# Performance work log

Measured on AMD Instinct MI355X. Metric: run time of the kernel, lower is better.

The kernel has to match this reference:

```python
import jax, jax.numpy as jnp
import numpy as np

G = 2048      # graphs
N = 48        # nodes per graph
NTOT = G * N  # 98304 total nodes
F_IN = 64
HID = 128
HEADS = 1
K = 4         # TopKPooling ratio (int -> k nodes per graph)
DEG = 8
E = NTOT * DEG
ATT = HEADS * 8  # attention pooling heads
EPS = 1e-5


def setup_inputs() -> dict:
    key = jax.random.key(0)
    ks = jax.random.split(key, 20)
    off = (jnp.arange(G, dtype=jnp.int32) * N)[:, None]
    # intra-graph random edges (source j -> target i), GATConv convention
    edge_src = (jax.random.randint(ks[0], (G, N * DEG), 0, N, dtype=jnp.int32) + off).reshape(-1)
    edge_dst = (jax.random.randint(ks[1], (G, N * DEG), 0, N, dtype=jnp.int32) + off).reshape(-1)
    batch = jnp.repeat(jnp.arange(G, dtype=jnp.int32), N)

    def w(k, shape, fan):
        return jax.random.normal(k, shape, jnp.float32) * (1.0 / np.sqrt(fan))

    HH = HEADS * HID
    return dict(
        x=jax.random.normal(ks[2], (NTOT, F_IN), jnp.float32),
        edge_src=edge_src, edge_dst=edge_dst, batch=batch,
        # GATConv 1/2/3: weight, att_src, att_dst, bias
        W1=w(ks[3], (F_IN, HH), F_IN), as1=w(ks[4], (HEADS, HID), HID), ad1=w(ks[5], (HEADS, HID), HID), b1=jnp.zeros((HH,), jnp.float32),
        W2=w(ks[6], (HH, HH), HH), as2=w(ks[7], (HEADS, HID), HID), ad2=w(ks[8], (HEADS, HID), HID), b2=jnp.zeros((HH,), jnp.float32),
        W3=w(ks[9], (HH, HH), HH), as3=w(ks[10], (HEADS, HID), HID), ad3=w(ks[11], (HEADS, HID), HID), b3=jnp.zeros((HID,), jnp.float32),
        ln1_w=jnp.ones((HH,), jnp.float32), ln1_b=jnp.zeros((HH,), jnp.float32),
        ln2_w=jnp.ones((HH,), jnp.float32), ln2_b=jnp.zeros((HH,), jnp.float32),
        ln3_w=jnp.ones((HID,), jnp.float32), ln3_b=jnp.zeros((HID,), jnp.float32),
        pool_w=w(ks[12], (HID,), HID),
        fc1_w=w(ks[13], (HID, HID), HID), fc1_b=jnp.zeros((HID,), jnp.float32),
        fc2_w=w(ks[14], (HID, ATT), HID), fc2_b=jnp.zeros((ATT,), jnp.float32),
    )


def _forward(x, edge_src, edge_dst, W1, as1, ad1, b1, W2, as2, ad2, b2,
             W3, as3, ad3, b3, ln1_w, ln1_b, ln2_w, ln2_b, ln3_w, ln3_b,
             pool_w, fc1_w, fc1_b, fc2_w, fc2_b):
    # GATConv adds self-loops
    loop = jnp.arange(NTOT, dtype=edge_src.dtype)
    src = jnp.concatenate([edge_src, loop])
    dst = jnp.concatenate([edge_dst, loop])

    def gat(h_in, W, a_s, a_d, bias, concat):
        H, C = a_s.shape
        h = (h_in @ W).reshape(NTOT, H, C)
        # e_ij = LeakyReLU(a_src . h_j + a_dst . h_i), softmax over incoming edges of i
        e = jax.nn.leaky_relu((h * a_s).sum(-1)[src] + (h * a_d).sum(-1)[dst], 0.2)  # [E', H]
        m = jax.ops.segment_max(e, dst, num_segments=NTOT)
        p = jnp.exp(e - m[dst])
        z = jax.ops.segment_sum(p, dst, num_segments=NTOT)
        alpha = p / (z[dst] + 1e-16)
        out = jax.ops.segment_sum(h[src] * alpha[:, :, None], dst, num_segments=NTOT)
        out = out.reshape(NTOT, H * C) if concat else out.mean(1)
        return out + bias

    def graph_ln(h, w, b):  # PyG LayerNorm mode='graph': normalize over nodes+channels per graph
        h3 = h.reshape(G, N, -1)
        mu = h3.mean((1, 2), keepdims=True)
        var = ((h3 - mu) ** 2).mean((1, 2), keepdims=True)
        return (((h3 - mu) / jnp.sqrt(var + EPS)) * w + b).reshape(NTOT, -1)

    h = jax.nn.relu(graph_ln(gat(x, W1, as1, ad1, b1, True), ln1_w, ln1_b))
    h = jax.nn.relu(graph_ln(gat(h, W2, as2, ad2, b2, True), ln2_w, ln2_b))
    h = graph_ln(gat(h, W3, as3, ad3, b3, False), ln3_w, ln3_b)  # [NTOT, HID]

    # TopKPooling: score = tanh(x.w/||w||), pick K nodes per graph, scale features by score
    score = jnp.tanh((h @ pool_w) / jnp.linalg.norm(pool_w))
    vals, idx = jax.lax.top_k(score.reshape(G, N), K)          # [G, K]
    h3 = h.reshape(G, N, HID)
    pooled = (jnp.take_along_axis(h3, idx[:, :, None], axis=1) * vals[:, :, None]).reshape(G, K * HID)

    # per-graph attention pooling (vectorized over the original Python loop)
    t = jnp.tanh(h3 @ fc1_w + fc1_b)                            # [G, N, HID]
    att = jax.nn.softmax(t @ fc2_w + fc2_b, axis=1)             # softmax over nodes, [G, N, ATT]
    emb = jnp.einsum('gna,gnh->gah', att, h3)                   # [G, ATT, HID]
    avg = emb.sum(-1) / ATT                                     # [G, ATT]

    return jnp.concatenate([pooled, avg], axis=1)               # [G, K*HID + ATT]


def reference(x, edge_src, edge_dst, batch, W1, as1, ad1, b1, W2, as2, ad2, b2,
              W3, as3, ad3, b3, ln1_w, ln1_b, ln2_w, ln2_b, ln3_w, ln3_b,
              pool_w, fc1_w, fc1_b, fc2_w, fc2_b):
    # batch is implicit in the uniform [G, N] layout; kept for signature fidelity
    del batch
    return _forward(x, edge_src, edge_dst, W1, as1, ad1, b1, W2, as2, ad2, b2,
                    W3, as3, ad3, b3, ln1_w, ln1_b, ln2_w, ln2_b, ln3_w, ln3_b,
                    pool_w, fc1_w, fc1_b, fc2_w, fc2_b)
```

## Files before the change

kernel.cpp:

```cpp
#include <hip/hip_runtime.h>
#include <math.h>

#define NG   2048
#define NN   48
#define FIN  64
#define HIDC 128
#define DEG  8
#define EPG  (NN*DEG)
#define NATT 8
#define KTOP 4
#define NTH  256
#define OUTW (KTOP*HIDC + NATT)

struct alignas(16) SM {
  float hA[NN*HIDC];
  float hB[NN*HIDC];
  float alpha[EPG];
  float ssrc[NN], sdst[NN], aself[NN];
  float rs[NN], sc[NN];
  float red[16];
  float valk[KTOP];
  int   idxk[KTOP];
  int   row_start[NN+1];
  int   fill[NN];
  unsigned char csr_src[EPG];
};

__device__ __forceinline__ float fast_tanh(float x) {
  float e = __expf(2.f * x);
  return 1.f - 2.f * __builtin_amdgcn_rcpf(e + 1.f);
}

template<int KD>
__device__ __forceinline__ void gemm48(const float* in, const float* __restrict__ W,
                                       int t, float acc[6][4]) {
  const int col = t & 31, row = t >> 5;
  const int c0 = col * 4, n0 = row * 6;
  #pragma unroll
  for (int i = 0; i < 6; ++i)
    #pragma unroll
    for (int j = 0; j < 4; ++j) acc[i][j] = 0.f;
  const float* wp = W + c0;
  float4 w0 = *(const float4*)(wp + 0*HIDC);
  float4 w1 = *(const float4*)(wp + 1*HIDC);
  float4 w2 = *(const float4*)(wp + 2*HIDC);
  float4 w3 = *(const float4*)(wp + 3*HIDC);
  #pragma unroll 2
  for (int kb = 0; kb < KD - 4; kb += 4) {
    const float* np = wp + (size_t)(kb + 4) * HIDC;
    float4 nw0 = *(const float4*)(np + 0*HIDC);
    float4 nw1 = *(const float4*)(np + 1*HIDC);
    float4 nw2 = *(const float4*)(np + 2*HIDC);
    float4 nw3 = *(const float4*)(np + 3*HIDC);
    #pragma unroll
    for (int i = 0; i < 6; ++i) {
      float4 h = *(const float4*)(in + (n0+i)*KD + kb);
      acc[i][0] = fmaf(h.w, w3.x, fmaf(h.z, w2.x, fmaf(h.y, w1.x, fmaf(h.x, w0.x, acc[i][0]))));
      acc[i][1] = fmaf(h.w, w3.y, fmaf(h.z, w2.y, fmaf(h.y, w1.y, fmaf(h.x, w0.y, acc[i][1]))));
      acc[i][2] = fmaf(h.w, w3.z, fmaf(h.z, w2.z, fmaf(h.y, w1.z, fmaf(h.x, w0.z, acc[i][2]))));
      acc[i][3] = fmaf(h.w, w3.w, fmaf(h.z, w2.w, fmaf(h.y, w1.w, fmaf(h.x, w0.w, acc[i][3]))));
    }
    w0 = nw0; w1 = nw1; w2 = nw2; w3 = nw3;
  }
  {
    const int kb = KD - 4;
    #pragma unroll
    for (int i = 0; i < 6; ++i) {
      float4 h = *(const float4*)(in + (n0+i)*KD + kb);
      acc[i][0] = fmaf(h.w, w3.x, fmaf(h.z, w2.x, fmaf(h.y, w1.x, fmaf(h.x, w0.x, acc[i][0]))));
      acc[i][1] = fmaf(h.w, w3.y, fmaf(h.z, w2.y, fmaf(h.y, w1.y, fmaf(h.x, w0.y, acc[i][1]))));
      acc[i][2] = fmaf(h.w, w3.z, fmaf(h.z, w2.z, fmaf(h.y, w1.z, fmaf(h.x, w0.z, acc[i][2]))));
      acc[i][3] = fmaf(h.w, w3.w, fmaf(h.z, w2.w, fmaf(h.y, w1.w, fmaf(h.x, w0.w, acc[i][3]))));
    }
  }
}

template<int KD, bool RELU>
__device__ __forceinline__ void gat_layer(SM& s, const float* in, float* hmid, float* outbuf,
                                          const float* __restrict__ W,
                                          const float* __restrict__ avs,
                                          const float* __restrict__ avd,
                                          const float* __restrict__ bias,
                                          const float* __restrict__ lnw,
                                          const float* __restrict__ lnb, int t) {
  float acc[6][4];
  gemm48<KD>(in, W, t, acc);
  const int col = t & 31, row = t >> 5, c0 = col * 4, n0 = row * 6;
  float4 asv = *(const float4*)(avs + c0);
  float4 adv = *(const float4*)(avd + c0);
  #pragma unroll
  for (int i = 0; i < 6; ++i) {
    float4 v = make_float4(acc[i][0], acc[i][1], acc[i][2], acc[i][3]);
    *(float4*)(hmid + (n0+i)*HIDC + c0) = v;
    float ps = v.x*asv.x + v.y*asv.y + v.z*asv.z + v.w*asv.w;
    float pd = v.x*adv.x + v.y*adv.y + v.z*adv.z + v.w*adv.w;
    #pragma unroll
    for (int off = 16; off > 0; off >>= 1) {
      ps += __shfl_xor(ps, off, 32);
      pd += __shfl_xor(pd, off, 32);
    }
    if (col == 0) { s.ssrc[n0+i] = ps; s.sdst[n0+i] = pd; }
  }
  __syncthreads();

  if (t < 4*NN) {
    const int n = t >> 2, l = t & 3;
    const int b0 = s.row_start[n], b1 = s.row_start[n+1];
    const float di = s.sdst[n];
    float es = s.ssrc[n] + di; es = es > 0.f ? es : 0.2f*es;
    float m = es;
    for (int q = b0 + l; q < b1; q += 4) {
      float e = s.ssrc[s.csr_src[q]] + di; e = e > 0.f ? e : 0.2f*e;
      s.alpha[q] = e;
      m = fmaxf(m, e);
    }
    m = fmaxf(m, __shfl_xor(m, 1, 4));
    m = fmaxf(m, __shfl_xor(m, 2, 4));
    float pself = expf(es - m);
    float z = (l == 0) ? pself : 0.f;
    for (int q = b0 + l; q < b1; q += 4) {
      float p = expf(s.alpha[q] - m); s.alpha[q] = p; z += p;
    }
    z += __shfl_xor(z, 1, 4);
    z += __shfl_xor(z, 2, 4);
    float inv = 1.f / (z + 1e-16f);
    for (int q = b0 + l; q < b1; q += 4) s.alpha[q] *= inv;
    if (l == 0) s.aself[n] = pself * inv;
  }
  __syncthreads();

  {
    const int cg = t & 31, rg = t >> 5;
    const float4 bc = *(const float4*)(bias + cg*4);
    const float4* hm4 = (const float4*)hmid;
    float4* ob4 = (float4*)outbuf;
    float lsum = 0.f, lsq = 0.f;
    #pragma unroll
    for (int j = 0; j < 6; ++j) {
      const int i = rg + 8*j;
      const int b0 = s.row_start[i], b1 = s.row_start[i+1];
      float4 hv = hm4[i*32 + cg];
      const float asf = s.aself[i];
      float4 av = make_float4(asf*hv.x, asf*hv.y, asf*hv.z, asf*hv.w);
      int q = b0;
      float a_nxt = 0.f; int s_nxt = 0;
      if (q < b1) { a_nxt = s.alpha[q]; s_nxt = s.csr_src[q]; }
      while (q < b1) {
        const float a = a_nxt; const int sc = s_nxt;
        ++q;
        if (q < b1) { a_nxt = s.alpha[q]; s_nxt = s.csr_src[q]; }
        float4 h4 = hm4[sc*32 + cg];
        av.x = fmaf(a, h4.x, av.x);
        av.y = fmaf(a, h4.y, av.y);
        av.z = fmaf(a, h4.z, av.z);
        av.w = fmaf(a, h4.w, av.w);
      }
      av.x += bc.x; av.y += bc.y; av.z += bc.z; av.w += bc.w;
      ob4[i*32 + cg] = av;
      lsum += av.x + av.y + av.z + av.w;
      lsq = fmaf(av.x, av.x, lsq); lsq = fmaf(av.y, av.y, lsq);
      lsq = fmaf(av.z, av.z, lsq); lsq = fmaf(av.w, av.w, lsq);
    }
    #pragma unroll
    for (int off = 32; off > 0; off >>= 1) {
      lsum += __shfl_xor(lsum, off, 64);
      lsq  += __shfl_xor(lsq,  off, 64);
    }
    const int wid = t >> 6;
    if ((t & 63) == 0) { s.red[wid] = lsum; s.red[8+wid] = lsq; }
  }
  __syncthreads();

  {
    float su = s.red[0] + s.red[1] + s.red[2] + s.red[3];
    float sq = s.red[8] + s.red[9] + s.red[10] + s.red[11];
    const float inv_n = 1.f / (NN*HIDC);
    const float mu = su * inv_n;
    const float rstd = 1.f / sqrtf(sq * inv_n - mu*mu + 1e-5f);
    const int cg = t & 31;
    const float4 wc  = *(const float4*)(lnw + cg*4);
    const float4 bcn = *(const float4*)(lnb + cg*4);
    float4* ob4 = (float4*)outbuf;
    for (int e = t; e < NN*32; e += NTH) {
      float4 v = ob4[e];
      v.x = (v.x - mu)*rstd*wc.x + bcn.x;
      v.y = (v.y - mu)*rstd*wc.y + bcn.y;
      v.z = (v.z - mu)*rstd*wc.z + bcn.z;
      v.w = (v.w - mu)*rstd*wc.w + bcn.w;
      if (RELU) {
        v.x = fmaxf(v.x, 0.f); v.y = fmaxf(v.y, 0.f);
        v.z = fmaxf(v.z, 0.f); v.w = fmaxf(v.w, 0.f);
      }
      ob4[e] = v;
    }
  }
  __syncthreads();
}

__global__ __launch_bounds__(NTH)
void gat_fused(const float* __restrict__ x,
               const int* __restrict__ edge_src, const int* __restrict__ edge_dst,
               const float* __restrict__ W1, const float* __restrict__ as1, const float* __restrict__ ad1, const float* __restrict__ b1,
               const float* __restrict__ W2, const float* __restrict__ as2, const float* __restrict__ ad2, const float* __restrict__ b2,
               const float* __restrict__ W3, const float* __restrict__ as3, const float* __restrict__ ad3, const float* __restrict__ b3,
               const float* __restrict__ ln1w, const float* __restrict__ ln1b,
               const float* __restrict__ ln2w, const float* __restrict__ ln2b,
               const float* __restrict__ ln3w, const float* __restrict__ ln3b,
               const float* __restrict__ poolw,
               const float* __restrict__ fc1w, const float* __restrict__ fc1b,
               const float* __restrict__ fc2w, const float* __restrict__ fc2b,
               float* __restrict__ out) {
  __shared__ SM s;
  const int g = blockIdx.x, t = threadIdx.x;
  const int base = g * NN;

  {
    const float4* xs = (const float4*)(x + (size_t)base*FIN);
    for (int e = t; e < NN*FIN/4; e += NTH) ((float4*)s.hA)[e] = xs[e];
  }

  if (t < NN) s.fill[t] = 0;
  __syncthreads();
  for (int e = t; e < EPG; e += NTH)
    atomicAdd(&s.fill[edge_dst[(size_t)g*EPG + e] - base], 1);
  __syncthreads();
  if (t < 64) {
    int cnt = (t < NN) ? s.fill[t] : 0;
    int xv = cnt;
    #pragma unroll
    for (int d = 1; d < 64; d <<= 1) {
      int v = __shfl_up(xv, d, 64);
      if (t >= d) xv += v;
    }
    if (t < NN) { s.row_start[t] = xv - cnt; s.fill[t] = xv - cnt; }
    if (t == NN-1) s.row_start[NN] = xv;
  }
  __syncthreads();
  for (int e = t; e < EPG; e += NTH) {
    int d  = edge_dst[(size_t)g*EPG + e] - base;
    int sl = edge_src[(size_t)g*EPG + e] - base;
    int pos = atomicAdd(&s.fill[d], 1);
    s.csr_src[pos] = (unsigned char)sl;
  }
  __syncthreads();

  gat_layer<FIN,  true >(s, s.hA, s.hB, s.hA, W1, as1, ad1, b1, ln1w, ln1b, t);
  gat_layer<HIDC, true >(s, s.hA, s.hB, s.hA, W2, as2, ad2, b2, ln2w, ln2b, t);
  gat_layer<HIDC, false>(s, s.hA, s.hB, s.hA, W3, as3, ad3, b3, ln3w, ln3b, t);

  float invnorm;
  {
    const int ln = t & 63;
    float p0 = poolw[ln], p1 = poolw[ln + 64];
    float v = p0*p0 + p1*p1;
    #pragma unroll
    for (int off = 32; off > 0; off >>= 1) v += __shfl_xor(v, off, 64);
    invnorm = 1.f / sqrtf(v);
  }

  {
    const int col = t & 31, row = t >> 5, n0 = row * 6;
    float pwv[4];
    #pragma unroll
    for (int q = 0; q < 4; ++q) pwv[q] = poolw[col + 32*q];
    #pragma unroll
    for (int i = 0; i < 6; ++i) {
      float d = 0.f, r = 0.f;
      #pragma unroll
      for (int q = 0; q < 4; ++q) {
        float v = s.hA[(n0+i)*HIDC + col + 32*q];
        d = fmaf(v, pwv[q], d); r += v;
      }
      #pragma unroll
      for (int off = 16; off > 0; off >>= 1) {
        d += __shfl_xor(d, off, 32);
        r += __shfl_xor(r, off, 32);
      }
      if (col == 0) { s.sc[n0+i] = tanhf(d * invnorm); s.rs[n0+i] = r; }
    }
  }
  __syncthreads();

  if (t < 64) {
    float cur = (t < NN) ? s.sc[t] : -1e30f;
    #pragma unroll
    for (int k = 0; k < KTOP; ++k) {
      float bv = cur; int bi = t;
      #pragma unroll
      for (int d = 1; d < 64; d <<= 1) {
        float ov = __shfl_xor(bv, d, 64);
        int   oi = __shfl_xor(bi, d, 64);
        if (ov > bv || (ov == bv && oi < bi)) { bv = ov; bi = oi; }
      }
      if (t == 0) { s.valk[k] = bv; s.idxk[k] = bi; }
      if (t == bi) cur = -1e30f;
    }
  }
  __syncthreads();

  float* og = out + (size_t)g * OUTW;
  for (int o = t; o < KTOP*HIDC; o += NTH) {
    int k = o >> 7, c = o & 127;
    og[o] = s.hA[s.idxk[k]*HIDC + c] * s.valk[k];
  }

  {
    float acc[6][4];
    gemm48<HIDC>(s.hA, fc1w, t, acc);
    const int col = t & 31, row = t >> 5, c0 = col*4, n0 = row*6;
    float4 bv = *(const float4*)(fc1b + c0);
    #pragma unroll
    for (int i = 0; i < 6; ++i) {
      float4 v;
      v.x = fast_tanh(acc[i][0] + bv.x); v.y = fast_tanh(acc[i][1] + bv.y);
      v.z = fast_tanh(acc[i][2] + bv.z); v.w = fast_tanh(acc[i][3] + bv.w);
      *(float4*)(s.hB + (n0+i)*HIDC + c0) = v;
    }
  }
  __syncthreads();

  {
    const int col = t & 31, row = t >> 5, n0 = row * 6;
    #pragma unroll
    for (int i = 0; i < 6; ++i) {
      float lg[NATT];
      #pragma unroll
      for (int a = 0; a < NATT; ++a) lg[a] = 0.f;
      #pragma unroll
      for (int q = 0; q < 4; ++q) {
        float v = s.hB[(n0+i)*HIDC + col + 32*q];
        const float* f2 = fc2w + (size_t)(col + 32*q)*NATT;
        #pragma unroll
        for (int a = 0; a < NATT; ++a) lg[a] = fmaf(v, f2[a], lg[a]);
      }
      #pragma unroll
      for (int a = 0; a < NATT; ++a) {
        #pragma unroll
        for (int off = 16; off > 0; off >>= 1) lg[a] += __shfl_xor(lg[a], off, 32);
      }
      if (col == 0) {
        #pragma unroll
        for (int a = 0; a < NATT; ++a) s.alpha[(n0+i)*NATT + a] = lg[a] + fc2b[a];
      }
    }
  }
  __syncthreads();

  {
    const int wv = t >> 6, ln = t & 63;
    #pragma unroll
    for (int aa = 0; aa < 2; ++aa) {
      const int a = wv + 4*aa;
      float lg = (ln < NN) ? s.alpha[ln*NATT + a] : -1e30f;
      float m = lg;
      #pragma unroll
      for (int off = 32; off > 0; off >>= 1) m = fmaxf(m, __shfl_xor(m, off, 64));
      float p = (ln < NN) ? expf(lg - m) : 0.f;
      float w_n = (ln < NN) ? s.rs[ln] : 0.f;
      float zz = p, acc0 = p * w_n;
      #pragma unroll
      for (int off = 32; off > 0; off >>= 1) {
        zz   += __shfl_xor(zz,   off, 64);
        acc0 += __shfl_xor(acc0, off, 64);
      }
      if (ln == 0) og[KTOP*HIDC + a] = acc0 / zz * (1.0f / NATT);
    }
  }
}

extern "C" void kernel_launch(void* const* d_in, const int* in_sizes, int n_in,
                              void* d_out, int out_size, void* d_ws, size_t ws_size,
                              hipStream_t stream) {
  (void)in_sizes; (void)n_in; (void)d_ws; (void)ws_size; (void)out_size;
  const float* x    = (const float*)d_in[0];
  const int*   esrc = (const int*)  d_in[1];
  const int*   edst = (const int*)  d_in[2];
  const float* W1   = (const float*)d_in[4];
  const float* as1  = (const float*)d_in[5];
  const float* ad1  = (const float*)d_in[6];
  const float* b1   = (const float*)d_in[7];
  const float* W2   = (const float*)d_in[8];
  const float* as2  = (const float*)d_in[9];
  const float* ad2  = (const float*)d_in[10];
  const float* b2   = (const float*)d_in[11];
  const float* W3   = (const float*)d_in[12];
  const float* as3  = (const float*)d_in[13];
  const float* ad3  = (const float*)d_in[14];
  const float* b3   = (const float*)d_in[15];
  const float* ln1w = (const float*)d_in[16];
  const float* ln1b = (const float*)d_in[17];
  const float* ln2w = (const float*)d_in[18];
  const float* ln2b = (const float*)d_in[19];
  const float* ln3w = (const float*)d_in[20];
  const float* ln3b = (const float*)d_in[21];
  const float* pw   = (const float*)d_in[22];
  const float* fc1w = (const float*)d_in[23];
  const float* fc1b = (const float*)d_in[24];
  const float* fc2w = (const float*)d_in[25];
  const float* fc2b = (const float*)d_in[26];
  float* out = (float*)d_out;

  gat_fused<<<NG, NTH, 0, stream>>>(x, esrc, edst,
                                    W1, as1, ad1, b1,
                                    W2, as2, ad2, b2,
                                    W3, as3, ad3, b3,
                                    ln1w, ln1b, ln2w, ln2b, ln3w, ln3b,
                                    pw, fc1w, fc1b, fc2w, fc2b, out);
}
```

Baseline: 246.2 us.

## Split fused GAT kernel into per-stage kernels with global workspace buffers

Replaces the single fused per-graph kernel, which held two 48x128 activation buffers in shared memory, with eight launches: CSR build, per-layer GEMM, per-layer aggregation+LayerNorm, and a pooling tail. Intermediates go through the workspace in global memory. Each kernel needs less LDS, so more blocks can be resident per CU. The cost is extra launches and global round-trips of the activations between stages. The old fused kernel is kept as a fallback when the workspace is too small.

```diff
diff --git a/kernel.cpp b/kernel.cpp
--- a/kernel.cpp
+++ b/kernel.cpp
@@ -11,6 +11,396 @@
 #define KTOP 4
 #define NTH  256
 #define OUTW (KTOP*HIDC + NATT)
+#define NTOT (NG*NN)
+
+__device__ __forceinline__ float fast_tanh(float x) {
+  float e = __expf(2.f * x);
+  return 1.f - 2.f * __builtin_amdgcn_rcpf(e + 1.f);
+}
+
+template<int KD>
+__device__ __forceinline__ void gemm48(const float* in, const float* __restrict__ W,
+                                       int t, float acc[6][4]) {
+  const int col = t & 31, row = t >> 5;
+  const int c0 = col * 4, n0 = row * 6;
+  #pragma unroll
+  for (int i = 0; i < 6; ++i)
+    #pragma unroll
+    for (int j = 0; j < 4; ++j) acc[i][j] = 0.f;
+  const float* wp = W + c0;
+  float4 w0 = *(const float4*)(wp + 0*HIDC);
+  float4 w1 = *(const float4*)(wp + 1*HIDC);
+  float4 w2 = *(const float4*)(wp + 2*HIDC);
+  float4 w3 = *(const float4*)(wp + 3*HIDC);
+  #pragma unroll 2
+  for (int kb = 0; kb < KD - 4; kb += 4) {
+    const float* np = wp + (size_t)(kb + 4) * HIDC;
+    float4 nw0 = *(const float4*)(np + 0*HIDC);
+    float4 nw1 = *(const float4*)(np + 1*HIDC);
+    float4 nw2 = *(const float4*)(np + 2*HIDC);
+    float4 nw3 = *(const float4*)(np + 3*HIDC);
+    #pragma unroll
+    for (int i = 0; i < 6; ++i) {
+      float4 h = *(const float4*)(in + (n0+i)*KD + kb);
+      acc[i][0] = fmaf(h.w, w3.x, fmaf(h.z, w2.x, fmaf(h.y, w1.x, fmaf(h.x, w0.x, acc[i][0]))));
+      acc[i][1] = fmaf(h.w, w3.y, fmaf(h.z, w2.y, fmaf(h.y, w1.y, fmaf(h.x, w0.y, acc[i][1]))));
+      acc[i][2] = fmaf(h.w, w3.z, fmaf(h.z, w2.z, fmaf(h.y, w1.z, fmaf(h.x, w0.z, acc[i][2]))));
+      acc[i][3] = fmaf(h.w, w3.w, fmaf(h.z, w2.w, fmaf(h.y, w1.w, fmaf(h.x, w0.w, acc[i][3]))));
+    }
+    w0 = nw0; w1 = nw1; w2 = nw2; w3 = nw3;
+  }
+  {
+    const int kb = KD - 4;
+    #pragma unroll
+    for (int i = 0; i < 6; ++i) {
+      float4 h = *(const float4*)(in + (n0+i)*KD + kb);
+      acc[i][0] = fmaf(h.w, w3.x, fmaf(h.z, w2.x, fmaf(h.y, w1.x, fmaf(h.x, w0.x, acc[i][0]))));
+      acc[i][1] = fmaf(h.w, w3.y, fmaf(h.z, w2.y, fmaf(h.y, w1.y, fmaf(h.x, w0.y, acc[i][1]))));
+      acc[i][2] = fmaf(h.w, w3.z, fmaf(h.z, w2.z, fmaf(h.y, w1.z, fmaf(h.x, w0.z, acc[i][2]))));
+      acc[i][3] = fmaf(h.w, w3.w, fmaf(h.z, w2.w, fmaf(h.y, w1.w, fmaf(h.x, w0.w, acc[i][3]))));
+    }
+  }
+}
+
+
+__global__ __launch_bounds__(64)
+void k_csr(const int* __restrict__ edge_src, const int* __restrict__ edge_dst,
+           int* __restrict__ grs, unsigned char* __restrict__ gcsr) {
+  __shared__ int fill[NN];
+  __shared__ int rstart[NN+1];
+  __shared__ unsigned char csr[EPG];
+  const int g = blockIdx.x, l = threadIdx.x, base = g*NN;
+  const int* ed = edge_dst + (size_t)g*EPG;
+  const int* es = edge_src + (size_t)g*EPG;
+  if (l < NN) fill[l] = 0;
+  __syncthreads();
+  #pragma unroll
+  for (int j = 0; j < EPG/64; ++j) atomicAdd(&fill[ed[j*64 + l] - base], 1);
+  __syncthreads();
+  {
+    int cnt = (l < NN) ? fill[l] : 0;
+    int xv = cnt;
+    #pragma unroll
+    for (int d = 1; d < 64; d <<= 1) {
+      int v = __shfl_up(xv, d, 64);
+      if (l >= d) xv += v;
+    }
+    if (l < NN) { rstart[l] = xv - cnt; fill[l] = xv - cnt; }
+    if (l == NN-1) rstart[NN] = xv;
+  }
+  __syncthreads();
+  #pragma unroll
+  for (int j = 0; j < EPG/64; ++j) {
+    int e = j*64 + l;
+    int pos = atomicAdd(&fill[ed[e] - base], 1);
+    csr[pos] = (unsigned char)(es[e] - base);
+  }
+  __syncthreads();
+  if (l < NN+1) grs[(size_t)g*(NN+1) + l] = rstart[l];
+  for (int j = l; j < EPG/4; j += 64)
+    ((int*)(gcsr + (size_t)g*EPG))[j] = ((const int*)csr)[j];
+}
+
+template<int KD>
+__global__ __launch_bounds__(NTH)
+void k_gemm(const float* __restrict__ hin, const float* __restrict__ W,
+            const float* __restrict__ avs, const float* __restrict__ avd,
+            float* __restrict__ msg, float* __restrict__ gss, float* __restrict__ gsd) {
+  __shared__ float hs[NN*KD];
+  const int g = blockIdx.x, t = threadIdx.x;
+  {
+    const float4* src = (const float4*)(hin + (size_t)g*NN*KD);
+    float4* dst = (float4*)hs;
+    #pragma unroll
+    for (int j = 0; j < (NN*KD/4)/NTH; ++j) dst[j*NTH + t] = src[j*NTH + t];
+  }
+  __syncthreads();
+  float acc[6][4];
+  gemm48<KD>(hs, W, t, acc);
+  const int col = t & 31, row = t >> 5, c0 = col*4, n0 = row*6;
+  float4 asv = *(const float4*)(avs + c0);
+  float4 adv = *(const float4*)(avd + c0);
+  float* mg = msg + (size_t)g*NN*HIDC;
+  #pragma unroll
+  for (int i = 0; i < 6; ++i) {
+    float4 v = make_float4(acc[i][0], acc[i][1], acc[i][2], acc[i][3]);
+    *(float4*)(mg + (n0+i)*HIDC + c0) = v;
+    float ps = v.x*asv.x + v.y*asv.y + v.z*asv.z + v.w*asv.w;
+    float pd = v.x*adv.x + v.y*adv.y + v.z*adv.z + v.w*adv.w;
+    #pragma unroll
+    for (int off = 16; off > 0; off >>= 1) {
+      ps += __shfl_xor(ps, off, 32);
+      pd += __shfl_xor(pd, off, 32);
+    }
+    if (col == 0) {
+      gss[(size_t)g*NN + n0+i] = ps;
+      gsd[(size_t)g*NN + n0+i] = pd;
+    }
+  }
+}
+
+template<bool RELU>
+__global__ __launch_bounds__(NTH)
+void k_agg(const float* __restrict__ msg,
+           const float* __restrict__ gss, const float* __restrict__ gsd,
+           const int* __restrict__ grs, const unsigned char* __restrict__ gcsr,
+           const float* __restrict__ bias,
+           const float* __restrict__ lnw, const float* __restrict__ lnb,
+           float* __restrict__ hout) {
+  __shared__ struct alignas(16) {
+    float m[NN*HIDC];
+    float alpha[EPG];
+    float ssrc[NN], sdst[NN], aself[NN];
+    float red[16];
+    int   row_start[NN+1];
+    unsigned char csr[EPG];
+  } s;
+  const int g = blockIdx.x, t = threadIdx.x;
+  {
+    const float4* src = (const float4*)(msg + (size_t)g*NN*HIDC);
+    float4* dst = (float4*)s.m;
+    #pragma unroll
+    for (int j = 0; j < (NN*HIDC/4)/NTH; ++j) dst[j*NTH + t] = src[j*NTH + t];
+  }
+  if (t < NN) { s.ssrc[t] = gss[(size_t)g*NN + t]; s.sdst[t] = gsd[(size_t)g*NN + t]; }
+  if (t >= 64 && t < 64 + NN + 1) s.row_start[t-64] = grs[(size_t)g*(NN+1) + (t-64)];
+  if (t >= 128 && t < 128 + EPG/4)
+    ((int*)s.csr)[t-128] = ((const int*)(gcsr + (size_t)g*EPG))[t-128];
+  __syncthreads();
+
+  if (t < 4*NN) {
+    const int n = t >> 2, l = t & 3;
+    const int b0 = s.row_start[n], b1 = s.row_start[n+1];
+    const float di = s.sdst[n];
+    float es = s.ssrc[n] + di; es = es > 0.f ? es : 0.2f*es;
+    float m = es;
+    for (int q = b0 + l; q < b1; q += 4) {
+      float e = s.ssrc[s.csr[q]] + di; e = e > 0.f ? e : 0.2f*e;
+      s.alpha[q] = e;
+      m = fmaxf(m, e);
+    }
+    m = fmaxf(m, __shfl_xor(m, 1, 4));
+    m = fmaxf(m, __shfl_xor(m, 2, 4));
+    float pself = expf(es - m);
+    float z = (l == 0) ? pself : 0.f;
+    for (int q = b0 + l; q < b1; q += 4) {
+      float p = expf(s.alpha[q] - m); s.alpha[q] = p; z += p;
+    }
+    z += __shfl_xor(z, 1, 4);
+    z += __shfl_xor(z, 2, 4);
+    float inv = 1.f / (z + 1e-16f);
+    for (int q = b0 + l; q < b1; q += 4) s.alpha[q] *= inv;
+    if (l == 0) s.aself[n] = pself * inv;
+  }
+  __syncthreads();
+
+  const int cg = t & 31, rg = t >> 5;
+  const float4 bc = *(const float4*)(bias + cg*4);
+  const float4* hm4 = (const float4*)s.m;
+  float4 av[6];
+  float lsum = 0.f, lsq = 0.f;
+  #pragma unroll
+  for (int j = 0; j < 6; ++j) {
+    const int i = rg + 8*j;
+    const int b0 = s.row_start[i], b1 = s.row_start[i+1];
+    float4 hv = hm4[i*32 + cg];
+    const float asf = s.aself[i];
+    float4 a4 = make_float4(asf*hv.x, asf*hv.y, asf*hv.z, asf*hv.w);
+    int q = b0;
+    float a_nxt = 0.f; int s_nxt = 0;
+    if (q < b1) { a_nxt = s.alpha[q]; s_nxt = s.csr[q]; }
+    while (q < b1) {
+      const float a = a_nxt; const int sc = s_nxt;
+      ++q;
+      if (q < b1) { a_nxt = s.alpha[q]; s_nxt = s.csr[q]; }
+      float4 h4 = hm4[sc*32 + cg];
+      a4.x = fmaf(a, h4.x, a4.x);
+      a4.y = fmaf(a, h4.y, a4.y);
+      a4.z = fmaf(a, h4.z, a4.z);
+      a4.w = fmaf(a, h4.w, a4.w);
+    }
+    a4.x += bc.x; a4.y += bc.y; a4.z += bc.z; a4.w += bc.w;
+    av[j] = a4;
+    lsum += a4.x + a4.y + a4.z + a4.w;
+    lsq = fmaf(a4.x, a4.x, lsq); lsq = fmaf(a4.y, a4.y, lsq);
+    lsq = fmaf(a4.z, a4.z, lsq); lsq = fmaf(a4.w, a4.w, lsq);
+  }
+  #pragma unroll
+  for (int off = 32; off > 0; off >>= 1) {
+    lsum += __shfl_xor(lsum, off, 64);
+    lsq  += __shfl_xor(lsq,  off, 64);
+  }
+  const int wid = t >> 6;
+  if ((t & 63) == 0) { s.red[wid] = lsum; s.red[8+wid] = lsq; }
+  __syncthreads();
+  {
+    float su = s.red[0] + s.red[1] + s.red[2] + s.red[3];
+    float sq = s.red[8] + s.red[9] + s.red[10] + s.red[11];
+    const float inv_n = 1.f / (NN*HIDC);
+    const float mu = su * inv_n;
+    const float rstd = 1.f / sqrtf(sq * inv_n - mu*mu + 1e-5f);
+    const float4 wc  = *(const float4*)(lnw + cg*4);
+    const float4 bcn = *(const float4*)(lnb + cg*4);
+    float4* ho = (float4*)(hout + (size_t)g*NN*HIDC);
+    #pragma unroll
+    for (int j = 0; j < 6; ++j) {
+      const int i = rg + 8*j;
+      float4 v = av[j];
+      v.x = (v.x - mu)*rstd*wc.x + bcn.x;
+      v.y = (v.y - mu)*rstd*wc.y + bcn.y;
+      v.z = (v.z - mu)*rstd*wc.z + bcn.z;
+      v.w = (v.w - mu)*rstd*wc.w + bcn.w;
+      if (RELU) {
+        v.x = fmaxf(v.x, 0.f); v.y = fmaxf(v.y, 0.f);
+        v.z = fmaxf(v.z, 0.f); v.w = fmaxf(v.w, 0.f);
+      }
+      ho[i*32 + cg] = v;
+    }
+  }
+}
+
+__global__ __launch_bounds__(NTH)
+void k_tail(const float* __restrict__ hbuf,
+            const float* __restrict__ poolw,
+            const float* __restrict__ fc1w, const float* __restrict__ fc1b,
+            const float* __restrict__ fc2w, const float* __restrict__ fc2b,
+            float* __restrict__ out) {
+  __shared__ struct alignas(16) {
+    float h[NN*HIDC];
+    float tb[NN*HIDC];
+    float logits[NN*NATT];
+    float rs[NN], sc[NN];
+    float valk[KTOP];
+    int   idxk[KTOP];
+  } s;
+  const int g = blockIdx.x, t = threadIdx.x;
+  {
+    const float4* src = (const float4*)(hbuf + (size_t)g*NN*HIDC);
+    float4* dst = (float4*)s.h;
+    #pragma unroll
+    for (int j = 0; j < (NN*HIDC/4)/NTH; ++j) dst[j*NTH + t] = src[j*NTH + t];
+  }
+  __syncthreads();
+
+  float invnorm;
+  {
+    const int ln = t & 63;
+    float p0 = poolw[ln], p1 = poolw[ln + 64];
+    float v = p0*p0 + p1*p1;
+    #pragma unroll
+    for (int off = 32; off > 0; off >>= 1) v += __shfl_xor(v, off, 64);
+    invnorm = 1.f / sqrtf(v);
+  }
+  {
+    const int col = t & 31, row = t >> 5, n0 = row * 6;
+    float pwv[4];
+    #pragma unroll
+    for (int q = 0; q < 4; ++q) pwv[q] = poolw[col + 32*q];
+    #pragma unroll
+    for (int i = 0; i < 6; ++i) {
+      float d = 0.f, r = 0.f;
+      #pragma unroll
+      for (int q = 0; q < 4; ++q) {
+        float v = s.h[(n0+i)*HIDC + col + 32*q];
+        d = fmaf(v, pwv[q], d); r += v;
+      }
+      #pragma unroll
+      for (int off = 16; off > 0; off >>= 1) {
+        d += __shfl_xor(d, off, 32);
+        r += __shfl_xor(r, off, 32);
+      }
+      if (col == 0) { s.sc[n0+i] = tanhf(d * invnorm); s.rs[n0+i] = r; }
+    }
+  }
+  __syncthreads();
+
+  if (t < 64) {
+    float cur = (t < NN) ? s.sc[t] : -1e30f;
+    #pragma unroll
+    for (int k = 0; k < KTOP; ++k) {
+      float bv = cur; int bi = t;
+      #pragma unroll
+      for (int d = 1; d < 64; d <<= 1) {
+        float ov = __shfl_xor(bv, d, 64);
+        int   oi = __shfl_xor(bi, d, 64);
+        if (ov > bv || (ov == bv && oi < bi)) { bv = ov; bi = oi; }
+      }
+      if (t == 0) { s.valk[k] = bv; s.idxk[k] = bi; }
+      if (t == bi) cur = -1e30f;
+    }
+  }
+  __syncthreads();
+
+  float* og = out + (size_t)g * OUTW;
+  for (int o = t; o < KTOP*HIDC; o += NTH) {
+    int k = o >> 7, c = o & 127;
+    og[o] = s.h[s.idxk[k]*HIDC + c] * s.valk[k];
+  }
+
+  {
+    float acc[6][4];
+    gemm48<HIDC>(s.h, fc1w, t, acc);
+    const int col = t & 31, row = t >> 5, c0 = col*4, n0 = row*6;
+    float4 bv = *(const float4*)(fc1b + c0);
+    #pragma unroll
+    for (int i = 0; i < 6; ++i) {
+      float4 v;
+      v.x = fast_tanh(acc[i][0] + bv.x); v.y = fast_tanh(acc[i][1] + bv.y);
+      v.z = fast_tanh(acc[i][2] + bv.z); v.w = fast_tanh(acc[i][3] + bv.w);
+      *(float4*)(s.tb + (n0+i)*HIDC + c0) = v;
+    }
+  }
+  __syncthreads();
+
+  {
+    const int col = t & 31, row = t >> 5, n0 = row * 6;
+    #pragma unroll
+    for (int i = 0; i < 6; ++i) {
+      float lg[NATT];
+      #pragma unroll
+      for (int a = 0; a < NATT; ++a) lg[a] = 0.f;
+      #pragma unroll
+      for (int q = 0; q < 4; ++q) {
+        float v = s.tb[(n0+i)*HIDC + col + 32*q];
+        const float* f2 = fc2w + (size_t)(col + 32*q)*NATT;
+        #pragma unroll
+        for (int a = 0; a < NATT; ++a) lg[a] = fmaf(v, f2[a], lg[a]);
+      }
+      #pragma unroll
+      for (int a = 0; a < NATT; ++a) {
+        #pragma unroll
+        for (int off = 16; off > 0; off >>= 1) lg[a] += __shfl_xor(lg[a], off, 32);
+      }
+      if (col == 0) {
+        #pragma unroll
+        for (int a = 0; a < NATT; ++a) s.logits[(n0+i)*NATT + a] = lg[a] + fc2b[a];
+      }
+    }
+  }
+  __syncthreads();
+
+  {
+    const int wv = t >> 6, ln = t & 63;
+    #pragma unroll
+    for (int aa = 0; aa < 2; ++aa) {
+      const int a = wv + 4*aa;
+      float lg = (ln < NN) ? s.logits[ln*NATT + a] : -1e30f;
+      float m = lg;
+      #pragma unroll
+      for (int off = 32; off > 0; off >>= 1) m = fmaxf(m, __shfl_xor(m, off, 64));
+      float p = (ln < NN) ? expf(lg - m) : 0.f;
+      float w_n = (ln < NN) ? s.rs[ln] : 0.f;
+      float zz = p, acc0 = p * w_n;
+      #pragma unroll
+      for (int off = 32; off > 0; off >>= 1) {
+        zz   += __shfl_xor(zz,   off, 64);
+        acc0 += __shfl_xor(acc0, off, 64);
+      }
+      if (ln == 0) og[KTOP*HIDC + a] = acc0 / zz * (1.0f / NATT);
+    }
+  }
+}
+
 
 struct alignas(16) SM {
   float hA[NN*HIDC];
@@ -25,55 +415,6 @@
   int   fill[NN];
   unsigned char csr_src[EPG];
 };
-
-__device__ __forceinline__ float fast_tanh(float x) {
-  float e = __expf(2.f * x);
-  return 1.f - 2.f * __builtin_amdgcn_rcpf(e + 1.f);
-}
-
-template<int KD>
-__device__ __forceinline__ void gemm48(const float* in, const float* __restrict__ W,
-                                       int t, float acc[6][4]) {
-  const int col = t & 31, row = t >> 5;
-  const int c0 = col * 4, n0 = row * 6;
-  #pragma unroll
-  for (int i = 0; i < 6; ++i)
-    #pragma unroll
-    for (int j = 0; j < 4; ++j) acc[i][j] = 0.f;
-  const float* wp = W + c0;
-  float4 w0 = *(const float4*)(wp + 0*HIDC);
-  float4 w1 = *(const float4*)(wp + 1*HIDC);
-  float4 w2 = *(const float4*)(wp + 2*HIDC);
-  float4 w3 = *(const float4*)(wp + 3*HIDC);
-  #pragma unroll 2
-  for (int kb = 0; kb < KD - 4; kb += 4) {
-    const float* np = wp + (size_t)(kb + 4) * HIDC;
-    float4 nw0 = *(const float4*)(np + 0*HIDC);
-    float4 nw1 = *(const float4*)(np + 1*HIDC);
-    float4 nw2 = *(const float4*)(np + 2*HIDC);
-    float4 nw3 = *(const float4*)(np + 3*HIDC);
-    #pragma unroll
-    for (int i = 0; i < 6; ++i) {
-      float4 h = *(const float4*)(in + (n0+i)*KD + kb);
-      acc[i][0] = fmaf(h.w, w3.x, fmaf(h.z, w2.x, fmaf(h.y, w1.x, fmaf(h.x, w0.x, acc[i][0]))));
-      acc[i][1] = fmaf(h.w, w3.y, fmaf(h.z, w2.y, fmaf(h.y, w1.y, fmaf(h.x, w0.y, acc[i][1]))));
-      acc[i][2] = fmaf(h.w, w3.z, fmaf(h.z, w2.z, fmaf(h.y, w1.z, fmaf(h.x, w0.z, acc[i][2]))));
-      acc[i][3] = fmaf(h.w, w3.w, fmaf(h.z, w2.w, fmaf(h.y, w1.w, fmaf(h.x, w0.w, acc[i][3]))));
-    }
-    w0 = nw0; w1 = nw1; w2 = nw2; w3 = nw3;
-  }
-  {
-    const int kb = KD - 4;
-    #pragma unroll
-    for (int i = 0; i < 6; ++i) {
-      float4 h = *(const float4*)(in + (n0+i)*KD + kb);
-      acc[i][0] = fmaf(h.w, w3.x, fmaf(h.z, w2.x, fmaf(h.y, w1.x, fmaf(h.x, w0.x, acc[i][0]))));
-      acc[i][1] = fmaf(h.w, w3.y, fmaf(h.z, w2.y, fmaf(h.y, w1.y, fmaf(h.x, w0.y, acc[i][1]))));
-      acc[i][2] = fmaf(h.w, w3.z, fmaf(h.z, w2.z, fmaf(h.y, w1.z, fmaf(h.x, w0.z, acc[i][2]))));
-      acc[i][3] = fmaf(h.w, w3.w, fmaf(h.z, w2.w, fmaf(h.y, w1.w, fmaf(h.x, w0.w, acc[i][3]))));
-    }
-  }
-}
 
 template<int KD, bool RELU>
 __device__ __forceinline__ void gat_layer(SM& s, const float* in, float* hmid, float* outbuf,
@@ -102,7 +443,6 @@
     if (col == 0) { s.ssrc[n0+i] = ps; s.sdst[n0+i] = pd; }
   }
   __syncthreads();
-
   if (t < 4*NN) {
     const int n = t >> 2, l = t & 3;
     const int b0 = s.row_start[n], b1 = s.row_start[n+1];
@@ -128,7 +468,6 @@
     if (l == 0) s.aself[n] = pself * inv;
   }
   __syncthreads();
-
   {
     const int cg = t & 31, rg = t >> 5;
     const float4 bc = *(const float4*)(bias + cg*4);
@@ -170,7 +509,6 @@
     if ((t & 63) == 0) { s.red[wid] = lsum; s.red[8+wid] = lsq; }
   }
   __syncthreads();
-
   {
     float su = s.red[0] + s.red[1] + s.red[2] + s.red[3];
     float sq = s.red[8] + s.red[9] + s.red[10] + s.red[11];
@@ -213,12 +551,10 @@
   __shared__ SM s;
   const int g = blockIdx.x, t = threadIdx.x;
   const int base = g * NN;
-
   {
     const float4* xs = (const float4*)(x + (size_t)base*FIN);
     for (int e = t; e < NN*FIN/4; e += NTH) ((float4*)s.hA)[e] = xs[e];
   }
-
   if (t < NN) s.fill[t] = 0;
   __syncthreads();
   for (int e = t; e < EPG; e += NTH)
@@ -257,7 +593,6 @@
     for (int off = 32; off > 0; off >>= 1) v += __shfl_xor(v, off, 64);
     invnorm = 1.f / sqrtf(v);
   }
-
   {
     const int col = t & 31, row = t >> 5, n0 = row * 6;
     float pwv[4];
@@ -280,7 +615,6 @@
     }
   }
   __syncthreads();
-
   if (t < 64) {
     float cur = (t < NN) ? s.sc[t] : -1e30f;
     #pragma unroll
@@ -303,7 +637,6 @@
     int k = o >> 7, c = o & 127;
     og[o] = s.hA[s.idxk[k]*HIDC + c] * s.valk[k];
   }
-
   {
     float acc[6][4];
     gemm48<HIDC>(s.hA, fc1w, t, acc);
@@ -318,7 +651,6 @@
     }
   }
   __syncthreads();
-
   {
     const int col = t & 31, row = t >> 5, n0 = row * 6;
     #pragma unroll
@@ -345,7 +677,6 @@
     }
   }
   __syncthreads();
-
   {
     const int wv = t >> 6, ln = t & 63;
     #pragma unroll
@@ -371,7 +702,7 @@
 extern "C" void kernel_launch(void* const* d_in, const int* in_sizes, int n_in,
                               void* d_out, int out_size, void* d_ws, size_t ws_size,
                               hipStream_t stream) {
-  (void)in_sizes; (void)n_in; (void)d_ws; (void)ws_size; (void)out_size;
+  (void)in_sizes; (void)n_in; (void)out_size;
   const float* x    = (const float*)d_in[0];
   const int*   esrc = (const int*)  d_in[1];
   const int*   edst = (const int*)  d_in[2];
@@ -400,10 +731,32 @@
   const float* fc2b = (const float*)d_in[26];
   float* out = (float*)d_out;
 
-  gat_fused<<<NG, NTH, 0, stream>>>(x, esrc, edst,
-                                    W1, as1, ad1, b1,
-                                    W2, as2, ad2, b2,
-                                    W3, as3, ad3, b3,
-                                    ln1w, ln1b, ln2w, ln2b, ln3w, ln3b,
-                                    pw, fc1w, fc1b, fc2w, fc2b, out);
-}
+  const size_t n_msg = (size_t)NTOT*HIDC;
+  const size_t need = (2*n_msg + 2*(size_t)NTOT) * sizeof(float)
+                    + (size_t)NG*(NN+1)*sizeof(int) + (size_t)NG*EPG + 256;
+  if (ws_size >= need) {
+    char* w = (char*)d_ws;
+    float* msg  = (float*)w;                      w += n_msg*sizeof(float);
+    float* hbuf = (float*)w;                      w += n_msg*sizeof(float);
+    float* gss  = (float*)w;                      w += (size_t)NTOT*sizeof(float);
+    float* gsd  = (float*)w;                      w += (size_t)NTOT*sizeof(float);
+    int*   grs  = (int*)w;                        w += (size_t)NG*(NN+1)*sizeof(int);
+    unsigned char* gcsr = (unsigned char*)w;
+
+    k_csr<<<NG, 64, 0, stream>>>(esrc, edst, grs, gcsr);
+    k_gemm<FIN ><<<NG, NTH, 0, stream>>>(x,    W1, as1, ad1, msg, gss, gsd);
+    k_agg<true ><<<NG, NTH, 0, stream>>>(msg, gss, gsd, grs, gcsr, b1, ln1w, ln1b, hbuf);
+    k_gemm<HIDC><<<NG, NTH, 0, stream>>>(hbuf, W2, as2, ad2, msg, gss, gsd);
+    k_agg<true ><<<NG, NTH, 0, stream>>>(msg, gss, gsd, grs, gcsr, b2, ln2w, ln2b, hbuf);
+    k_gemm<HIDC><<<NG, NTH, 0, stream>>>(hbuf, W3, as3, ad3, msg, gss, gsd);
+    k_agg<false><<<NG, NTH, 0, stream>>>(msg, gss, gsd, grs, gcsr, b3, ln3w, ln3b, hbuf);
+    k_tail<<<NG, NTH, 0, stream>>>(hbuf, pw, fc1w, fc1b, fc2w, fc2b, out);
+  } else {
+    gat_fused<<<NG, NTH, 0, stream>>>(x, esrc, edst,
+                                      W1, as1, ad1, b1,
+                                      W2, as2, ad2, b2,
+                                      W3, as3, ad3, b3,
+                                      ln1w, ln1b, ln2w, ln2b, ln3w, ln3b,
+                                      pw, fc1w, fc1b, fc2w, fc2b, out);
+  }
+}
```

New measurement: 307.5 us. +24.9%, slower.
